# Kernel optimization log

Measured on AMD Instinct MI355X. Metric: run time of the kernel, lower is better.

Reference implementation:

```python
import jax, jax.numpy as jnp
import numpy as np

B, C = 32768, 1000
EPS = 1e-6

def setup_inputs() -> dict:
    key = jax.random.key(0)
    k1, k2 = jax.random.split(key)
    # p_tar / p_vlm are probability distributions over C classes
    p_tar = jax.nn.softmax(jax.random.normal(k1, (B, C), dtype=jnp.float32), axis=1)
    p_vlm = jax.nn.softmax(jax.random.normal(k2, (B, C), dtype=jnp.float32), axis=1)
    alpha = jnp.array([0.99], dtype=jnp.float32)  # EMA momentum
    memory_bank = jnp.full((C, C), 1.0 / C, dtype=jnp.float32)  # __init__ state
    return {"p_tar": p_tar, "p_vlm": p_vlm, "alpha": alpha, "memory_bank": memory_bank}

def _uncertainty(p):
    return -p * jnp.log(p + EPS)

def reference(p_tar, p_vlm, alpha, memory_bank):
    n_classes = memory_bank.shape[0]
    norm = 1.0 / jnp.sqrt(jnp.float32(n_classes))
    # --- class_prototype_atten (uses PRE-update memory bank, as in torch) ---
    atten = jax.nn.softmax(jnp.matmul(p_tar, memory_bank.T) * norm, axis=1)  # [B, C]
    p_tar_new = jnp.matmul(atten, memory_bank)  # [B, C]
    # --- update_membank: vectorized per-class masked-mean EMA ---
    y_tar = jnp.argmax(p_tar, axis=1)
    y_vlm = jnp.argmax(p_vlm, axis=1)
    agree = y_tar == y_vlm
    # non-agreeing rows dumped into extra segment n_classes
    seg = jnp.where(agree, y_tar, n_classes)
    sums = jax.ops.segment_sum(p_tar, seg, num_segments=n_classes + 1)[:n_classes]  # [C, C]
    counts = jax.ops.segment_sum(agree.astype(p_tar.dtype), seg, num_segments=n_classes + 1)[:n_classes]  # [C]
    has = counts > 0
    mean = sums / jnp.where(has, counts, 1.0)[:, None]
    a = alpha.reshape(())
    bank_new = jnp.where(has[:, None], a * memory_bank + (1.0 - a) * mean, memory_bank)
    # --- uncertainty_mixing ---
    eu_tar = jnp.exp(-_uncertainty(p_tar_new))
    eu_vlm = jnp.exp(-_uncertainty(p_vlm))
    p_mix = (eu_tar * p_tar_new + eu_vlm * p_vlm) / (eu_tar + eu_vlm)
    return p_mix, bank_new
```

## Files before the change

### kernel.cpp

```cpp
#include <hip/hip_runtime.h>
#include <hip/hip_bf16.h>
#include <cstdint>
#include <cstddef>

#define NROWS 32768
#define NCLS  1000
#define KP    1024
#define NCH   32

typedef unsigned short u16;
typedef __bf16 bf16x8 __attribute__((ext_vector_type(8)));
typedef float  f32x4  __attribute__((ext_vector_type(4)));


__device__ __forceinline__ void gld_lds16(const u16* g, u16* l) {
  __builtin_amdgcn_global_load_lds(
      (const __attribute__((address_space(1))) unsigned int*)g,
      (__attribute__((address_space(3))) unsigned int*)l, 16, 0, 0);
}

__global__ __launch_bounds__(128)
void prep4_bank(const float* __restrict__ bank,
                __hip_bfloat16* __restrict__ M4,
                __hip_bfloat16* __restrict__ MT4) {
  __shared__ float tile[32][33];
  const int tx = blockIdx.x;
  const int ty = blockIdx.y;
  const int t  = threadIdx.x;
  {
    const int r = t >> 2, c0 = (t & 3) * 8;
    const int gj = ty * 32 + r;
    #pragma unroll
    for (int j = 0; j < 8; ++j) {
      const int gk = tx * 32 + c0 + j;
      tile[r][c0 + j] = (gj < NCLS && gk < NCLS) ? bank[gj * NCLS + gk] : 0.0f;
    }
  }
  __syncthreads();
  const int w = t >> 6, lane = t & 63, lr = lane & 15, qq = lane >> 4;
  if (w == 0) {
    #pragma unroll
    for (int s = 0; s < 2; ++s) {
      bf16x8 o;
      #pragma unroll
      for (int j = 0; j < 8; ++j) o[j] = (__bf16)tile[s * 16 + lr][qq * 8 + j];
      *(bf16x8*)((u16*)M4 + ((size_t)(ty * 2 + s) * NCH + tx) * 512 + lane * 8) = o;
    }
  } else {
    #pragma unroll
    for (int s = 0; s < 2; ++s) {
      bf16x8 o;
      #pragma unroll
      for (int j = 0; j < 8; ++j) o[j] = (__bf16)tile[qq * 8 + j][s * 16 + lr];
      *(bf16x8*)((u16*)MT4 + ((size_t)(tx * 2 + s) * NCH + ty) * 512 + lane * 8) = o;
    }
  }
}

__global__ __launch_bounds__(256)
void rows4_kernel(const float* __restrict__ p_tar, const float* __restrict__ p_vlm,
                  __hip_bfloat16* __restrict__ A4,
                  float* __restrict__ sums, float* __restrict__ counts) {
  const int w = threadIdx.x >> 6, lane = threadIdx.x & 63;
  const int lr = lane & 15, q = lane >> 4;
  const int panel = blockIdx.x * 4 + w;
  const int row   = panel * 16 + lr;
  const float* tr = p_tar + (size_t)row * NCLS;
  const float* vr = p_vlm + (size_t)row * NCLS;
  u16* a4 = (u16*)A4 + (size_t)panel * NCH * 512 + lane * 8;

  float bvT = -1.0f; int biT = 0;
  float bvV = -1.0f; int biV = 0;
  for (int c = 0; c < NCH; ++c) {
    const int k0 = c * 32 + q * 8;
    float v[8];
    if (k0 < NCLS) {
      float4 x = *(const float4*)(tr + k0);
      float4 y = *(const float4*)(tr + k0 + 4);
      v[0] = x.x; v[1] = x.y; v[2] = x.z; v[3] = x.w;
      v[4] = y.x; v[5] = y.y; v[6] = y.z; v[7] = y.w;
    } else {
      #pragma unroll
      for (int j = 0; j < 8; ++j) v[j] = 0.0f;
    }
    bf16x8 o;
    #pragma unroll
    for (int j = 0; j < 8; ++j) {
      o[j] = (__bf16)v[j];
      if (v[j] > bvT) { bvT = v[j]; biT = k0 + j; }
    }
    *(bf16x8*)(a4 + (size_t)c * 512) = o;
    if (k0 < NCLS) {
      float4 x = *(const float4*)(vr + k0);
      float4 y = *(const float4*)(vr + k0 + 4);
      float u[8] = {x.x, x.y, x.z, x.w, y.x, y.y, y.z, y.w};
      #pragma unroll
      for (int j = 0; j < 8; ++j)
        if (u[j] > bvV) { bvV = u[j]; biV = k0 + j; }
    }
  }
  #pragma unroll
  for (int d = 16; d < 64; d <<= 1) {
    float ov = __shfl_xor(bvT, d); int oi = __shfl_xor(biT, d);
    if (ov > bvT || (ov == bvT && oi < biT)) { bvT = ov; biT = oi; }
    float ov2 = __shfl_xor(bvV, d); int oi2 = __shfl_xor(biV, d);
    if (ov2 > bvV || (ov2 == bvV && oi2 < biV)) { bvV = ov2; biV = oi2; }
  }
  const int ag = (biT == biV) ? 1 : 0;
  for (int rr = 0; rr < 16; ++rr) {
    const int agr = __shfl(ag, rr);
    if (agr) {
      const int cls = __shfl(biT, rr);
      const float* trr = p_tar + (size_t)(panel * 16 + rr) * NCLS;
      for (int k = lane; k < NCLS; k += 64)
        atomicAdd(&sums[(size_t)cls * NCLS + k], trr[k]);
      if (lane == 0) atomicAdd(&counts[cls], 1.0f);
    }
  }
}

template <int WHICH>
__global__ __launch_bounds__(256, 4)
void gemm4(const u16* __restrict__ A4, const u16* __restrict__ B4,
           __hip_bfloat16* __restrict__ E4out, float* __restrict__ rowsum,
           const float* __restrict__ p_vlm, float* __restrict__ mix_out) {
  __shared__ u16 SH[4][4096];
  const int tid  = threadIdx.x;
  const int w    = tid >> 6;
  const int lane = tid & 63;
  const int lr   = lane & 15;
  const int q    = lane >> 4;
  const int L    = blockIdx.y * 8 + blockIdx.x;
  const int bm   = L & 255;
  const int bn   = L >> 8;
  const int wm   = w >> 1;
  const int wn   = w & 1;

  f32x4 acc[4][4] = {};

  const u16* ga0 = A4 + ((size_t)(bm * 8 + 2 * w) * NCH) * 512 + lane * 8;
  const u16* ga1 = ga0 + (size_t)NCH * 512;
  const u16* gb0 = B4 + ((size_t)(bn * 8 + 2 * w) * NCH) * 512 + lane * 8;
  const u16* gb1 = gb0 + (size_t)NCH * 512;

  gld_lds16(ga0, &SH[0][(2 * w + 0) * 512]);
  gld_lds16(ga1, &SH[0][(2 * w + 1) * 512]);
  gld_lds16(gb0, &SH[2][(2 * w + 0) * 512]);
  gld_lds16(gb1, &SH[2][(2 * w + 1) * 512]);

  for (int i = 0; i < NCH; ++i) {
    const int cur = i & 1;
    __syncthreads();
    if (i + 1 < NCH) {
      const int nxt = cur ^ 1;
      const size_t ko = (size_t)(i + 1) * 512;
      gld_lds16(ga0 + ko, &SH[nxt][(2 * w + 0) * 512]);
      gld_lds16(ga1 + ko, &SH[nxt][(2 * w + 1) * 512]);
      gld_lds16(gb0 + ko, &SH[2 + nxt][(2 * w + 0) * 512]);
      gld_lds16(gb1 + ko, &SH[2 + nxt][(2 * w + 1) * 512]);
    }
    bf16x8 af[4], bfr[4];
    #pragma unroll
    for (int t = 0; t < 4; ++t) {
      af[t]  = *(const bf16x8*)(&SH[cur][(wm * 4 + t) * 512 + lane * 8]);
      bfr[t] = *(const bf16x8*)(&SH[2 + cur][(wn * 4 + t) * 512 + lane * 8]);
    }
    #pragma unroll
    for (int mt = 0; mt < 4; ++mt)
      #pragma unroll
      for (int nt = 0; nt < 4; ++nt)
        acc[mt][nt] = __builtin_amdgcn_mfma_f32_16x16x32_bf16(af[mt], bfr[nt], acc[mt][nt], 0, 0, 0);
  }

  const float NORM = 0.03162277660168379f;
  if (WHICH == 1) {
    __syncthreads();
    u16* ep = &SH[w][0];
    #pragma unroll
    for (int mt = 0; mt < 4; ++mt) {
      float psum[4] = {0.f, 0.f, 0.f, 0.f};
      #pragma unroll
      for (int nt = 0; nt < 4; ++nt) {
        const int gn = bn * 128 + wn * 64 + nt * 16 + lr;
        const int cc = nt >> 1;
        const int q2 = (nt & 1) * 2 + (lr >> 3);
        const int jj = lr & 7;
        #pragma unroll
        for (int r = 0; r < 4; ++r) {
          float e = (gn < NCLS) ? __expf(acc[mt][nt][r] * NORM) : 0.0f;
          psum[r] += e;
          __hip_bfloat16 h = __float2bfloat16(e);
          ep[(mt * 2 + cc) * 512 + (q2 * 16 + q * 4 + r) * 8 + jj] = *(u16*)&h;
        }
      }
      #pragma unroll
      for (int r = 0; r < 4; ++r) {
        float s = psum[r];
        s += __shfl_xor(s, 1); s += __shfl_xor(s, 2);
        s += __shfl_xor(s, 4); s += __shfl_xor(s, 8);
        if (lr == 0) atomicAdd(&rowsum[bm * 128 + wm * 64 + mt * 16 + q * 4 + r], s);
      }
    }
    #pragma unroll
    for (int ch = 0; ch < 8; ++ch) {
      const int mt = ch >> 1, cc = ch & 1;
      bf16x8 v = *(const bf16x8*)(&ep[ch * 512 + lane * 8]);
      const size_t Rg = bm * 8 + wm * 4 + mt;
      const size_t cg = bn * 4 + wn * 2 + cc;
      *(bf16x8*)((u16*)E4out + (Rg * NCH + cg) * 512 + lane * 8) = v;
    }
  } else {
    #pragma unroll
    for (int mt = 0; mt < 4; ++mt) {
      #pragma unroll
      for (int r = 0; r < 4; ++r) {
        const int gm = bm * 128 + wm * 64 + mt * 16 + q * 4 + r;
        const float inv = 1.0f / rowsum[gm];
        #pragma unroll
        for (int nt = 0; nt < 4; ++nt) {
          const int gn = bn * 128 + wn * 64 + nt * 16 + lr;
          if (gn < NCLS) {
            float pt = acc[mt][nt][r] * inv;
            float pv = p_vlm[(size_t)gm * NCLS + gn];
            float et = __expf(pt * __logf(pt + 1e-6f));
            float ev = __expf(pv * __logf(pv + 1e-6f));
            mix_out[(size_t)gm * NCLS + gn] = (et * pt + ev * pv) / (et + ev);
          }
        }
      }
    }
  }
}

__global__ __launch_bounds__(256)
void bank_update(const float* __restrict__ bank, const float* __restrict__ sums,
                 const float* __restrict__ counts, const float* __restrict__ alpha,
                 float* __restrict__ out) {
  const int idx = blockIdx.x * 256 + threadIdx.x;
  if (idx >= NCLS * NCLS) return;
  const int r = idx / NCLS;
  const float cnt = counts[r];
  const float bv  = bank[idx];
  const float a   = alpha[0];
  out[idx] = (cnt > 0.0f) ? a * bv + (1.0f - a) * (sums[idx] / cnt) : bv;
}

extern "C" void kernel_launch(void* const* d_in, const int* in_sizes, int n_in,
                              void* d_out, int out_size, void* d_ws, size_t ws_size,
                              hipStream_t stream) {
  const float* p_tar = (const float*)d_in[0];
  const float* p_vlm = (const float*)d_in[1];
  const float* alpha = (const float*)d_in[2];
  const float* bank  = (const float*)d_in[3];
  float* out_mix  = (float*)d_out;
  float* out_bank = (float*)d_out + (size_t)NROWS * NCLS;

  char* w = (char*)d_ws;
  __hip_bfloat16* A4  = (__hip_bfloat16*)w; w += (size_t)NROWS * KP * 2;
  __hip_bfloat16* E4  = (__hip_bfloat16*)w; w += (size_t)NROWS * KP * 2;
  __hip_bfloat16* M4  = (__hip_bfloat16*)w; w += (size_t)KP * KP * 2;
  __hip_bfloat16* MT4 = (__hip_bfloat16*)w; w += (size_t)KP * KP * 2;
  float* sums   = (float*)w;                w += (size_t)NCLS * NCLS * 4;
  float* counts = (float*)w;                w += 1024 * 4;
  float* rs     = (float*)w;                w += (size_t)NROWS * 4;

  hipMemsetAsync(sums, 0, (size_t)NCLS * NCLS * 4 + 1024 * 4 + (size_t)NROWS * 4, stream);

  prep4_bank<<<dim3(32, 32), 128, 0, stream>>>(bank, M4, MT4);
  rows4_kernel<<<NROWS / 64, 256, 0, stream>>>(p_tar, p_vlm, A4, sums, counts);
  gemm4<1><<<dim3(8, 256), 256, 0, stream>>>(
      (const u16*)A4, (const u16*)M4, E4, rs, nullptr, nullptr);
  gemm4<2><<<dim3(8, 256), 256, 0, stream>>>(
      (const u16*)E4, (const u16*)MT4, nullptr, rs, p_vlm, out_mix);
  bank_update<<<(NCLS * NCLS + 255) / 256, 256, 0, stream>>>(bank, sums, counts, alpha, out_bank);
}
```

Baseline: 598.2 us.

## Load GEMM B fragments directly from global and remap blocks per XCD

B operand fragments now come straight from global memory (L2-resident bank matrix) into registers instead of being staged through LDS, which halves LDS traffic and the async copies per iteration. Block indices are also remapped so that each XCD handles a contiguous range of row tiles with all eight column tiles, improving L2 locality for the A operand. The trade-off is exposed global-load latency for B inside the K loop, since there is no prefetch, and higher register pressure.

```diff
diff --git a/kernel.cpp b/kernel.cpp
--- a/kernel.cpp
+++ b/kernel.cpp
@@ -130,9 +130,11 @@
   const int lane = tid & 63;
   const int lr   = lane & 15;
   const int q    = lane >> 4;
-  const int L    = blockIdx.y * 8 + blockIdx.x;
-  const int bm   = L & 255;
-  const int bn   = L >> 8;
+  const int L    = blockIdx.x;
+  const int xcd  = L & 7;
+  const int jj   = L >> 3;
+  const int bm   = xcd * 32 + (jj >> 3);
+  const int bn   = jj & 7;
   const int wm   = w >> 1;
   const int wn   = w & 1;
 
@@ -140,31 +142,33 @@
 
   const u16* ga0 = A4 + ((size_t)(bm * 8 + 2 * w) * NCH) * 512 + lane * 8;
   const u16* ga1 = ga0 + (size_t)NCH * 512;
-  const u16* gb0 = B4 + ((size_t)(bn * 8 + 2 * w) * NCH) * 512 + lane * 8;
+  const u16* gb0 = B4 + ((size_t)(bn * 8 + wn * 4 + 0) * NCH) * 512 + lane * 8;
   const u16* gb1 = gb0 + (size_t)NCH * 512;
+  const u16* gb2 = gb1 + (size_t)NCH * 512;
+  const u16* gb3 = gb2 + (size_t)NCH * 512;
 
   gld_lds16(ga0, &SH[0][(2 * w + 0) * 512]);
   gld_lds16(ga1, &SH[0][(2 * w + 1) * 512]);
-  gld_lds16(gb0, &SH[2][(2 * w + 0) * 512]);
-  gld_lds16(gb1, &SH[2][(2 * w + 1) * 512]);
 
   for (int i = 0; i < NCH; ++i) {
     const int cur = i & 1;
+    const size_t kc = (size_t)i * 512;
     __syncthreads();
     if (i + 1 < NCH) {
       const int nxt = cur ^ 1;
-      const size_t ko = (size_t)(i + 1) * 512;
+      const size_t ko = kc + 512;
       gld_lds16(ga0 + ko, &SH[nxt][(2 * w + 0) * 512]);
       gld_lds16(ga1 + ko, &SH[nxt][(2 * w + 1) * 512]);
-      gld_lds16(gb0 + ko, &SH[2 + nxt][(2 * w + 0) * 512]);
-      gld_lds16(gb1 + ko, &SH[2 + nxt][(2 * w + 1) * 512]);
-    }
-    bf16x8 af[4], bfr[4];
-    #pragma unroll
-    for (int t = 0; t < 4; ++t) {
-      af[t]  = *(const bf16x8*)(&SH[cur][(wm * 4 + t) * 512 + lane * 8]);
-      bfr[t] = *(const bf16x8*)(&SH[2 + cur][(wn * 4 + t) * 512 + lane * 8]);
-    }
+    }
+    bf16x8 bfr[4];
+    bfr[0] = *(const bf16x8*)(gb0 + kc);
+    bfr[1] = *(const bf16x8*)(gb1 + kc);
+    bfr[2] = *(const bf16x8*)(gb2 + kc);
+    bfr[3] = *(const bf16x8*)(gb3 + kc);
+    bf16x8 af[4];
+    #pragma unroll
+    for (int t = 0; t < 4; ++t)
+      af[t] = *(const bf16x8*)(&SH[cur][(wm * 4 + t) * 512 + lane * 8]);
     #pragma unroll
     for (int mt = 0; mt < 4; ++mt)
       #pragma unroll
@@ -184,13 +188,13 @@
         const int gn = bn * 128 + wn * 64 + nt * 16 + lr;
         const int cc = nt >> 1;
         const int q2 = (nt & 1) * 2 + (lr >> 3);
-        const int jj = lr & 7;
+        const int jj2 = lr & 7;
         #pragma unroll
         for (int r = 0; r < 4; ++r) {
           float e = (gn < NCLS) ? __expf(acc[mt][nt][r] * NORM) : 0.0f;
           psum[r] += e;
           __hip_bfloat16 h = __float2bfloat16(e);
-          ep[(mt * 2 + cc) * 512 + (q2 * 16 + q * 4 + r) * 8 + jj] = *(u16*)&h;
+          ep[(mt * 2 + cc) * 512 + (q2 * 16 + q * 4 + r) * 8 + jj2] = *(u16*)&h;
         }
       }
       #pragma unroll
@@ -268,9 +272,9 @@
 
   prep4_bank<<<dim3(32, 32), 128, 0, stream>>>(bank, M4, MT4);
   rows4_kernel<<<NROWS / 64, 256, 0, stream>>>(p_tar, p_vlm, A4, sums, counts);
-  gemm4<1><<<dim3(8, 256), 256, 0, stream>>>(
+  gemm4<1><<<2048, 256, 0, stream>>>(
       (const u16*)A4, (const u16*)M4, E4, rs, nullptr, nullptr);
-  gemm4<2><<<dim3(8, 256), 256, 0, stream>>>(
+  gemm4<2><<<2048, 256, 0, stream>>>(
       (const u16*)E4, (const u16*)MT4, nullptr, rs, p_vlm, out_mix);
   bank_update<<<(NCLS * NCLS + 255) / 256, 256, 0, stream>>>(bank, sums, counts, alpha, out_bank);
 }
```

Measured after the change: 583.6 us. 1.03x faster.
